# Kernel optimization log

Measured on AMD Instinct MI355X. Metric: run time of the kernel, lower is better.

## Reference

```python
import jax, jax.numpy as jnp
import numpy as np

N_NODES = 50000


def _gcn_conv(x, row, col, W, b, n_nodes):
    # symmetric-norm GCN conv with self loops already appended to (row, col)
    deg = jax.ops.segment_sum(jnp.ones_like(row, dtype=x.dtype), row, num_segments=n_nodes)
    # every node has a self loop, so deg >= 1; pow(-0.5) is finite
    dis = deg ** -0.5
    norm = dis[row] * dis[col]                       # [E']
    msg = x[row] * norm[:, None]                     # gather + scale  [E', d]
    agg = jax.ops.segment_sum(msg, col, num_segments=n_nodes)  # scatter-add [N, d]
    return agg @ W + b


def setup_inputs() -> dict:
    key = jax.random.key(0)
    ks = jax.random.split(key, 12)
    N, E, Q, d_in, h = N_NODES, 800000, 200000, 64, 128
    x = jax.random.normal(ks[0], (N, d_in), dtype=jnp.float32)
    edge_index = jax.random.randint(ks[1], (2, E), 0, N)
    edge_label_index = jax.random.randint(ks[2], (2, Q), 0, N)
    def lin(k, fan_in, fan_out):
        kw, kb = jax.random.split(k)
        bound = 1.0 / np.sqrt(fan_in)
        W = jax.random.uniform(kw, (fan_in, fan_out), minval=-bound, maxval=bound, dtype=jnp.float32)
        b = jax.random.uniform(kb, (fan_out,), minval=-bound, maxval=bound, dtype=jnp.float32)
        return W, b
    W1, b1 = lin(ks[3], d_in, h)
    W2, b2 = lin(ks[4], h, h)
    Wc1, bc1 = lin(ks[5], 2 * h, h)
    Wc2, bc2 = lin(ks[6], h, 1)
    return {"x": x, "edge_index": edge_index, "edge_label_index": edge_label_index,
            "W1": W1, "b1": b1, "W2": W2, "b2": b2,
            "Wc1": Wc1, "bc1": bc1, "Wc2": Wc2, "bc2": bc2}


def reference(x, edge_index, edge_label_index, W1, b1, W2, b2, Wc1, bc1, Wc2, bc2):
    n = x.shape[0]
    loops = jnp.arange(n, dtype=edge_index.dtype)
    row = jnp.concatenate([edge_index[0], loops])
    col = jnp.concatenate([edge_index[1], loops])
    h1 = jax.nn.relu(_gcn_conv(x, row, col, W1, b1, n))
    h2 = _gcn_conv(h1, row, col, W2, b2, n)
    src, dst = edge_label_index[0], edge_label_index[1]
    h = jnp.concatenate([h2[src], h2[dst]], axis=1)  # [Q, 2*hidden]
    h = jax.nn.relu(h @ Wc1 + bc1)
    return h @ Wc2 + bc2                              # [Q, 1]
```

## Files before the change

kernel.cpp:

```cpp
#include <hip/hip_runtime.h>


#define HB 64
#define NWIN 16384

typedef __attribute__((ext_vector_type(8))) short short8;
typedef __attribute__((ext_vector_type(4))) float floatx4;

static __device__ __forceinline__ unsigned int f2bf(float v) {
    union { float f; unsigned int u; } c; c.f = v;
    unsigned int lsb = (c.u >> 16) & 1u;
    c.u += 0x7FFFu + lsb;
    return c.u >> 16;
}
static __device__ __forceinline__ float bf2f(unsigned int h) {
    union { float f; unsigned int u; } c; c.u = h << 16;
    return c.f;
}

__global__ __launch_bounds__(256) void k_pre(const int* __restrict__ row,
                                             const int* __restrict__ col,
                                             unsigned int* __restrict__ hRow,
                                             unsigned int* __restrict__ hCol,
                                             const float* __restrict__ x,
                                             unsigned int* __restrict__ xb,
                                             const float* __restrict__ W1,
                                             const float* __restrict__ W2,
                                             const float* __restrict__ Wc1,
                                             const float* __restrict__ b2,
                                             const float* __restrict__ bc1,
                                             unsigned short* __restrict__ UVhi,
                                             unsigned short* __restrict__ UVlo,
                                             unsigned short* __restrict__ W1hi,
                                             unsigned short* __restrict__ W1lo,
                                             float* __restrict__ buv,
                                             int E, int N, int W, int chunk,
                                             int nHist, int nXb) {
    __shared__ unsigned int lds[NWIN];
    int t = threadIdx.x, b = blockIdx.x;
    if (b < nHist) {
        int hb = b % HB;
        int yb = b / HB;
        int p = yb >> 1, win = yb & 1;
        int base = win * NWIN;
        int wcap = min(W - base, NWIN);
        if (wcap <= 0) return;
        const int* idxArr = p ? col : row;
        unsigned int* outArr = p ? hCol : hRow;
        int e0 = hb * chunk, e1 = min(E, e0 + chunk);
        for (int i = t; i < wcap; i += 256) lds[i] = 0;
        __syncthreads();
        for (int e = e0 + t; e < e1; e += 256) {
            int idx = idxArr[e];
            int w = (idx >> 1) - base;
            if ((unsigned)w < (unsigned)wcap)
                atomicAdd(&lds[w], 1u << ((idx & 1) * 16));
        }
        __syncthreads();
        for (int i = t; i < wcap; i += 256)
            outArr[(size_t)hb * W + base + i] = lds[i];
    } else if (b < nHist + nXb) {
        int i = (b - nHist) * 256 + t;
        if (i < N * 32) {
            float2 v = ((const float2*)x)[i];
            xb[i] = f2bf(v.x) | (f2bf(v.y) << 16);
        }
    } else {
        int bf = b - nHist - nXb;
        float* w2row = (float*)lds;
        if (bf < 128) {
            int k = bf;
            int j = t & 127, half = t >> 7;
            int n = half * 128 + j;
            const float* wc = Wc1 + (size_t)half * 128 * 128 + j;
            if (t < 128) w2row[t] = W2[k * 128 + t];
            __syncthreads();
            float acc = 0.f;
#pragma unroll 8
            for (int m = 0; m < 128; m++) acc += w2row[m] * wc[(size_t)m * 128];
            int kstep = k >> 5, kl = k & 31, quad = kl >> 3, j8 = kl & 7;
            int nb = n >> 4, l = quad * 16 + (n & 15);
            int pidx = ((kstep * 16 + nb) * 64 + l) * 8 + j8;
            unsigned int h = f2bf(acc);
            UVhi[pidx] = (unsigned short)h;
            UVlo[pidx] = (unsigned short)f2bf(acc - bf2f(h));
        } else if (bf == 128) {
            int j = t & 127, half = t >> 7;
            const float* wc = Wc1 + (size_t)half * 128 * 128 + j;
            float acc = half ? 0.f : bc1[j];
#pragma unroll 8
            for (int m = 0; m < 128; m++) acc += b2[m] * wc[(size_t)m * 128];
            buv[half * 128 + j] = acc;
        } else {
            int idx = (bf - 129) * 256 + t;
            int k = idx >> 7, n = idx & 127;
            float v = W1[k * 128 + n];
            int kstep = k >> 5, kl = k & 31, quad = kl >> 3, j8 = kl & 7;
            int nb = n >> 4, l = quad * 16 + (n & 15);
            int pidx = ((kstep * 8 + nb) * 64 + l) * 8 + j8;
            unsigned int h = f2bf(v);
            W1hi[pidx] = (unsigned short)h;
            W1lo[pidx] = (unsigned short)f2bf(v - bf2f(h));
        }
    }
}

__global__ __launch_bounds__(256) void k_rs(const unsigned int* __restrict__ hRow,
                                            unsigned int* __restrict__ hCol,
                                            float* __restrict__ dis,
                                            int* __restrict__ offs,
                                            int* __restrict__ bsum,
                                            int N, int W) {
    __shared__ int ts[256];
    int t = threadIdx.x;
    int w = blockIdx.x * 256 + t;
    unsigned int r0 = 0, r1 = 0, c0 = 0, c1 = 0;
    if (w < W) {
#pragma unroll 8
        for (int b = 0; b < HB; b++) {
            size_t idx = (size_t)b * W + w;
            unsigned int hr = hRow[idx];
            unsigned int hc = hCol[idx];
            hCol[idx] = c0 | (c1 << 16);
            r0 += hr & 0xFFFFu; r1 += hr >> 16;
            c0 += hc & 0xFFFFu; c1 += hc >> 16;
        }
        int n0 = 2 * w, n1 = 2 * w + 1;
        dis[n0] = 1.0f / sqrtf((float)(r0 + 1));
        if (n1 < N) dis[n1] = 1.0f / sqrtf((float)(r1 + 1));
    }
    int sum = (w < W) ? (int)(c0 + c1) : 0;
    ts[t] = sum;
    __syncthreads();
    for (int off = 1; off < 256; off <<= 1) {
        int xv = (t >= off) ? ts[t - off] : 0;
        __syncthreads();
        ts[t] += xv;
        __syncthreads();
    }
    int e = ts[t] - sum;
    if (w < W) {
        int n0 = 2 * w, n1 = 2 * w + 1;
        offs[n0] = e;
        if (n1 < N) offs[n1] = e + (int)c0;
    }
    if (t == 255) bsum[blockIdx.x] = ts[255];
}

__global__ __launch_bounds__(256) void k_scan2(int* __restrict__ bsum, int B) {
    __shared__ int ts[256];
    int t = threadIdx.x;
    int v = (t < B) ? bsum[t] : 0;
    ts[t] = v;
    __syncthreads();
    for (int off = 1; off < 256; off <<= 1) {
        int x = (t >= off) ? ts[t - off] : 0;
        __syncthreads();
        ts[t] += x;
        __syncthreads();
    }
    if (t < B) bsum[t] = ts[t] - v;
}

__global__ __launch_bounds__(256) void k_scan3(int* __restrict__ offs,
                                               const int* __restrict__ bsum,
                                               int N, int E) {
    int i = blockIdx.x * 256 + threadIdx.x;
    if (i < N) offs[i] = offs[i] + bsum[i >> 9];
    if (i == 0) offs[N] = E;
}

__global__ __launch_bounds__(256) void k_fill3(const int* __restrict__ row,
                                               const int* __restrict__ col,
                                               const int* __restrict__ offs,
                                               const unsigned int* __restrict__ hCol,
                                               int* __restrict__ srcSorted,
                                               int E, int N, int W, int chunk) {
    __shared__ int base[NWIN];
    int t = threadIdx.x, b = blockIdx.x;
    int n0 = blockIdx.y * NWIN;
    int nCnt = min(NWIN, N - n0);
    int e0 = b * chunk, e1 = min(E, e0 + chunk);
    for (int wl = t; wl * 2 < nCnt; wl += 256) {
        unsigned int pref = hCol[(size_t)b * W + (n0 >> 1) + wl];
        int nn = n0 + wl * 2;
        base[wl * 2] = offs[nn] + (int)(pref & 0xFFFFu);
        if (wl * 2 + 1 < nCnt)
            base[wl * 2 + 1] = offs[nn + 1] + (int)(pref >> 16);
    }
    __syncthreads();
    for (int e = e0 + t; e < e1; e += 256) {
        int c = col[e] - n0;
        if ((unsigned)c < (unsigned)nCnt) {
            int pos = atomicAdd(&base[c], 1);
            srcSorted[pos] = row[e];
        }
    }
}

__global__ __launch_bounds__(256) void k_conv1(const unsigned short* __restrict__ s,
                                               const int* __restrict__ offs,
                                               const int* __restrict__ srcs,
                                               const float* __restrict__ dis,
                                               const unsigned short* __restrict__ Bhi,
                                               const unsigned short* __restrict__ Blo,
                                               const float* __restrict__ b1,
                                               unsigned short* __restrict__ h1b, int N) {
    __shared__ unsigned short Ahi[16][72];
    __shared__ unsigned short Alo[16][72];
    int t = threadIdx.x;
    int lane = t & 63, wave = t >> 6;
    int quad = lane >> 4;
    short8 bh[2][2], bl[2][2];
#pragma unroll
    for (int ks = 0; ks < 2; ks++)
#pragma unroll
        for (int nt = 0; nt < 2; nt++) {
            int nb = wave * 2 + nt;
            bh[ks][nt] = *(const short8*)(Bhi + ((ks * 8 + nb) * 64 + lane) * 8);
            bl[ks][nt] = *(const short8*)(Blo + ((ks * 8 + nb) * 64 + lane) * 8);
        }
    {
        int nl = t >> 4;
        int node = blockIdx.x * 16 + nl;
        if (node < N) {
            int c4 = (t & 15) * 4;
            int e = offs[node], eEnd = offs[node + 1];
            float dn = dis[node];
            uint2 w = *(const uint2*)(s + (size_t)node * 64 + c4);
            float4 acc;
            acc.x = bf2f(w.x & 0xFFFF) * dn; acc.y = bf2f(w.x >> 16) * dn;
            acc.z = bf2f(w.y & 0xFFFF) * dn; acc.w = bf2f(w.y >> 16) * dn;
            while (e + 1 < eEnd) {
                int sA = srcs[e], sB = srcs[e + 1];
                float dA = dis[sA], dB = dis[sB];
                uint2 vA = *(const uint2*)(s + (size_t)sA * 64 + c4);
                uint2 vB = *(const uint2*)(s + (size_t)sB * 64 + c4);
                acc.x += bf2f(vA.x & 0xFFFF) * dA + bf2f(vB.x & 0xFFFF) * dB;
                acc.y += bf2f(vA.x >> 16) * dA + bf2f(vB.x >> 16) * dB;
                acc.z += bf2f(vA.y & 0xFFFF) * dA + bf2f(vB.y & 0xFFFF) * dB;
                acc.w += bf2f(vA.y >> 16) * dA + bf2f(vB.y >> 16) * dB;
                e += 2;
            }
            if (e < eEnd) {
                int sA = srcs[e];
                float dA = dis[sA];
                uint2 vA = *(const uint2*)(s + (size_t)sA * 64 + c4);
                acc.x += bf2f(vA.x & 0xFFFF) * dA; acc.y += bf2f(vA.x >> 16) * dA;
                acc.z += bf2f(vA.y & 0xFFFF) * dA; acc.w += bf2f(vA.y >> 16) * dA;
            }
            acc.x *= dn; acc.y *= dn; acc.z *= dn; acc.w *= dn;
            unsigned int h0 = f2bf(acc.x), h1 = f2bf(acc.y),
                         h2 = f2bf(acc.z), h3 = f2bf(acc.w);
            uint2 hw; hw.x = h0 | (h1 << 16); hw.y = h2 | (h3 << 16);
            uint2 lw;
            lw.x = f2bf(acc.x - bf2f(h0)) | (f2bf(acc.y - bf2f(h1)) << 16);
            lw.y = f2bf(acc.z - bf2f(h2)) | (f2bf(acc.w - bf2f(h3)) << 16);
            *(uint2*)(&Ahi[nl][c4]) = hw;
            *(uint2*)(&Alo[nl][c4]) = lw;
        }
    }
    __syncthreads();
    int ml = lane & 15;
    floatx4 acc[2] = {};
#pragma unroll
    for (int ks = 0; ks < 2; ks++) {
        short8 ahi = *(const short8*)(&Ahi[ml][ks * 32 + quad * 8]);
        short8 alo = *(const short8*)(&Alo[ml][ks * 32 + quad * 8]);
#pragma unroll
        for (int nt = 0; nt < 2; nt++) {
            acc[nt] = __builtin_amdgcn_mfma_f32_16x16x32_bf16(ahi, bh[ks][nt], acc[nt], 0, 0, 0);
            acc[nt] = __builtin_amdgcn_mfma_f32_16x16x32_bf16(ahi, bl[ks][nt], acc[nt], 0, 0, 0);
            acc[nt] = __builtin_amdgcn_mfma_f32_16x16x32_bf16(alo, bh[ks][nt], acc[nt], 0, 0, 0);
        }
    }
    int md = blockIdx.x * 16 + quad * 4;
#pragma unroll
    for (int nt = 0; nt < 2; nt++) {
        int n0 = (wave * 2 + nt) * 16 + (lane & 15);
        float bias = b1[n0];
#pragma unroll
        for (int r = 0; r < 4; r++) {
            int node = md + r;
            if (node < N)
                h1b[(size_t)node * 128 + n0] =
                    (unsigned short)f2bf(fmaxf(acc[nt][r] + bias, 0.f) * dis[node]);
        }
    }
}

__global__ __launch_bounds__(512) void k_conv2(const unsigned short* __restrict__ s,
                                               const int* __restrict__ offs,
                                               const int* __restrict__ srcs,
                                               const float* __restrict__ dis,
                                               const unsigned short* __restrict__ Bhi,
                                               const unsigned short* __restrict__ Blo,
                                               const float* __restrict__ buv,
                                               unsigned short* __restrict__ Ub,
                                               unsigned short* __restrict__ Vb, int N) {
    __shared__ unsigned short Ab[32][136];
    int t = threadIdx.x;
    {
        int nl = t >> 4;
        int node = blockIdx.x * 32 + nl;
        int c8 = (t & 15) * 8;
        if (node < N) {
            int e = offs[node], eEnd = offs[node + 1];
            float dn = dis[node];
            uint4 w = *(const uint4*)(s + (size_t)node * 128 + c8);
            float a0 = bf2f(w.x & 0xFFFF), a1 = bf2f(w.x >> 16);
            float a2 = bf2f(w.y & 0xFFFF), a3 = bf2f(w.y >> 16);
            float a4 = bf2f(w.z & 0xFFFF), a5 = bf2f(w.z >> 16);
            float a6 = bf2f(w.w & 0xFFFF), a7 = bf2f(w.w >> 16);
            while (e + 1 < eEnd) {
                int sA = srcs[e], sB = srcs[e + 1];
                uint4 vA = *(const uint4*)(s + (size_t)sA * 128 + c8);
                uint4 vB = *(const uint4*)(s + (size_t)sB * 128 + c8);
                a0 += bf2f(vA.x & 0xFFFF) + bf2f(vB.x & 0xFFFF);
                a1 += bf2f(vA.x >> 16) + bf2f(vB.x >> 16);
                a2 += bf2f(vA.y & 0xFFFF) + bf2f(vB.y & 0xFFFF);
                a3 += bf2f(vA.y >> 16) + bf2f(vB.y >> 16);
                a4 += bf2f(vA.z & 0xFFFF) + bf2f(vB.z & 0xFFFF);
                a5 += bf2f(vA.z >> 16) + bf2f(vB.z >> 16);
                a6 += bf2f(vA.w & 0xFFFF) + bf2f(vB.w & 0xFFFF);
                a7 += bf2f(vA.w >> 16) + bf2f(vB.w >> 16);
                e += 2;
            }
            if (e < eEnd) {
                int sA = srcs[e];
                uint4 vA = *(const uint4*)(s + (size_t)sA * 128 + c8);
                a0 += bf2f(vA.x & 0xFFFF); a1 += bf2f(vA.x >> 16);
                a2 += bf2f(vA.y & 0xFFFF); a3 += bf2f(vA.y >> 16);
                a4 += bf2f(vA.z & 0xFFFF); a5 += bf2f(vA.z >> 16);
                a6 += bf2f(vA.w & 0xFFFF); a7 += bf2f(vA.w >> 16);
            }
            uint4 o;
            o.x = f2bf(a0 * dn) | (f2bf(a1 * dn) << 16);
            o.y = f2bf(a2 * dn) | (f2bf(a3 * dn) << 16);
            o.z = f2bf(a4 * dn) | (f2bf(a5 * dn) << 16);
            o.w = f2bf(a6 * dn) | (f2bf(a7 * dn) << 16);
            *(uint4*)(&Ab[nl][c8]) = o;
        } else {
            uint4 z; z.x = 0; z.y = 0; z.z = 0; z.w = 0;
            *(uint4*)(&Ab[nl][c8]) = z;
        }
    }
    int lane = t & 63, wave = t >> 6, quad = lane >> 4, ml = lane & 15;
    short8 bh[4][2], bl[4][2];
#pragma unroll
    for (int ks = 0; ks < 4; ks++)
#pragma unroll
        for (int nt = 0; nt < 2; nt++) {
            int nb = wave * 2 + nt;
            bh[ks][nt] = *(const short8*)(Bhi + ((ks * 16 + nb) * 64 + lane) * 8);
            bl[ks][nt] = *(const short8*)(Blo + ((ks * 16 + nb) * 64 + lane) * 8);
        }
    __syncthreads();
#pragma unroll
    for (int g = 0; g < 2; g++) {
        int mbase = blockIdx.x * 32 + g * 16;
        floatx4 acc[2] = {};
#pragma unroll
        for (int ks = 0; ks < 4; ks++) {
            short8 a = *(const short8*)(&Ab[g * 16 + ml][ks * 32 + quad * 8]);
#pragma unroll
            for (int nt = 0; nt < 2; nt++) {
                acc[nt] = __builtin_amdgcn_mfma_f32_16x16x32_bf16(a, bh[ks][nt], acc[nt], 0, 0, 0);
                acc[nt] = __builtin_amdgcn_mfma_f32_16x16x32_bf16(a, bl[ks][nt], acc[nt], 0, 0, 0);
            }
        }
        int md = mbase + quad * 4;
#pragma unroll
        for (int nt = 0; nt < 2; nt++) {
            int n0 = (wave * 2 + nt) * 16 + ml;
            float bias = buv[n0];
            unsigned short* dst = (n0 < 128) ? Ub : Vb;
            int cc = n0 & 127;
#pragma unroll
            for (int r = 0; r < 4; r++) {
                int nd = md + r;
                if (nd < N)
                    dst[(size_t)nd * 128 + cc] =
                        (unsigned short)f2bf(acc[nt][r] + bias);
            }
        }
    }
}

__global__ __launch_bounds__(256) void k_head(const unsigned short* __restrict__ Ub,
                                              const unsigned short* __restrict__ Vb,
                                              const int* __restrict__ srcA,
                                              const int* __restrict__ dstA,
                                              const float* __restrict__ Wc2,
                                              const float* __restrict__ bc2,
                                              float* __restrict__ out, int Q) {
    int t = threadIdx.x;
    int q = blockIdx.x * 16 + (t >> 4);
    if (q >= Q) return;
    int l = t & 15;
    int s = srcA[q], d = dstA[q];
    uint4 u = *(const uint4*)(Ub + (size_t)s * 128 + l * 8);
    uint4 v = *(const uint4*)(Vb + (size_t)d * 128 + l * 8);
    const float4* w = (const float4*)(Wc2 + l * 8);
    float4 w0 = w[0], w1 = w[1];
    float acc = 0.f, z;
    z = fmaxf(bf2f(u.x & 0xFFFF) + bf2f(v.x & 0xFFFF), 0.f); acc += z * w0.x;
    z = fmaxf(bf2f(u.x >> 16)    + bf2f(v.x >> 16),    0.f); acc += z * w0.y;
    z = fmaxf(bf2f(u.y & 0xFFFF) + bf2f(v.y & 0xFFFF), 0.f); acc += z * w0.z;
    z = fmaxf(bf2f(u.y >> 16)    + bf2f(v.y >> 16),    0.f); acc += z * w0.w;
    z = fmaxf(bf2f(u.z & 0xFFFF) + bf2f(v.z & 0xFFFF), 0.f); acc += z * w1.x;
    z = fmaxf(bf2f(u.z >> 16)    + bf2f(v.z >> 16),    0.f); acc += z * w1.y;
    z = fmaxf(bf2f(u.w & 0xFFFF) + bf2f(v.w & 0xFFFF), 0.f); acc += z * w1.z;
    z = fmaxf(bf2f(u.w >> 16)    + bf2f(v.w >> 16),    0.f); acc += z * w1.w;
    acc += __shfl_xor(acc, 1);
    acc += __shfl_xor(acc, 2);
    acc += __shfl_xor(acc, 4);
    acc += __shfl_xor(acc, 8);
    if (l == 0) out[q] = acc + bc2[0];
}

extern "C" void kernel_launch(void* const* d_in, const int* in_sizes, int n_in,
                              void* d_out, int out_size, void* d_ws, size_t ws_size,
                              hipStream_t stream) {
    const float* x   = (const float*)d_in[0];
    const int*   ei  = (const int*)d_in[1];
    const int*   eli = (const int*)d_in[2];
    const float* W1  = (const float*)d_in[3];
    const float* b1  = (const float*)d_in[4];
    const float* W2  = (const float*)d_in[5];
    const float* b2  = (const float*)d_in[6];
    const float* Wc1 = (const float*)d_in[7];
    const float* bc1 = (const float*)d_in[8];
    const float* Wc2 = (const float*)d_in[9];
    const float* bc2 = (const float*)d_in[10];
    float* out = (float*)d_out;
    char* wsb = (char*)d_ws;

    const int N = in_sizes[0] / 64;
    const int E = in_sizes[1] / 2;
    const int Q = in_sizes[2] / 2;
    const int W = (N + 1) / 2;
    const int chunk = (E + HB - 1) / HB;
    const int nPass = (N + NWIN - 1) / NWIN;
    const int nWinH = (W + NWIN - 1) / NWIN;
    const int nHist = HB * 2 * nWinH;
    const int nXb   = (N * 32 + 255) / 256;
    const int rsB   = (W + 255) / 256;

    float* dis       = (float*)wsb;
    int*   offs      = (int*)wsb + 65536;
    int*   bsum      = (int*)wsb + 197120;
    float* buv       = (float*)wsb + 262912;
    unsigned short* UVhi = (unsigned short*)((int*)wsb + 263168);
    unsigned short* UVlo = (unsigned short*)((int*)wsb + 279552);
    unsigned short* W1hi = (unsigned short*)((int*)wsb + 295936);
    unsigned short* W1lo = (unsigned short*)((int*)wsb + 300032);
    int*   srcSorted = (int*)wsb + 304128;
    unsigned short* Vb   = (unsigned short*)((int*)wsb + 1104128);
    unsigned short* h1b  = (unsigned short*)((int*)wsb + 4304128);
    unsigned short* Ub   = (unsigned short*)((int*)wsb + 7504128);
    unsigned int* hRow = (unsigned int*)wsb + 10704128;
    unsigned int* hCol = (unsigned int*)wsb + 12304128;
    unsigned int* xb   = (unsigned int*)wsb + 13904128;

    const int* row  = ei;
    const int* col  = ei + E;
    const int* srcA = eli;
    const int* dstA = eli + Q;

    k_pre<<<nHist + nXb + 161, 256, 0, stream>>>(
        row, col, hRow, hCol, x, xb, W1, W2, Wc1, b2, bc1,
        UVhi, UVlo, W1hi, W1lo, buv, E, N, W, chunk, nHist, nXb);
    k_rs<<<rsB, 256, 0, stream>>>(hRow, hCol, dis, offs, bsum, N, W);
    k_scan2<<<1, 256, 0, stream>>>(bsum, rsB);
    k_scan3<<<(N + 255) / 256, 256, 0, stream>>>(offs, bsum, N, E);
    k_fill3<<<dim3(HB, nPass), 256, 0, stream>>>(row, col, offs, hCol, srcSorted, E, N, W, chunk);
    k_conv1<<<(N + 15) / 16, 256, 0, stream>>>(
        (const unsigned short*)xb, offs, srcSorted, dis, W1hi, W1lo, b1, h1b, N);
    k_conv2<<<(N + 31) / 32, 512, 0, stream>>>(
        h1b, offs, srcSorted, dis, UVhi, UVlo, buv, Ub, Vb, N);
    k_head<<<(Q + 15) / 16, 256, 0, stream>>>(Ub, Vb, srcA, dstA, Wc2, bc2, out, Q);
}
```

Before: 257.9 us.

## Split conv2 neighbor gather across two half-warps and unroll gather loops by four

In conv2, each node's edge list is now split between two 16-lane groups that take alternating edges and combine their sums with a cross-lane shuffle. Each block handles 16 nodes instead of 32, so twice as many blocks launch. Conv1's gather loop is also unrolled to four edges per iteration. The goal is more gather loads in flight, to hide latency on the memory-bound aggregation. The cost is that each block loads the same B fragments from global memory twice as often, and work is duplicated when a node has few edges.

```diff
diff --git a/kernel.cpp b/kernel.cpp
--- a/kernel.cpp
+++ b/kernel.cpp
@@ -231,6 +231,23 @@
             float4 acc;
             acc.x = bf2f(w.x & 0xFFFF) * dn; acc.y = bf2f(w.x >> 16) * dn;
             acc.z = bf2f(w.y & 0xFFFF) * dn; acc.w = bf2f(w.y >> 16) * dn;
+            while (e + 3 < eEnd) {
+                int sA = srcs[e], sB = srcs[e + 1], sC = srcs[e + 2], sD = srcs[e + 3];
+                float dA = dis[sA], dB = dis[sB], dC = dis[sC], dD = dis[sD];
+                uint2 vA = *(const uint2*)(s + (size_t)sA * 64 + c4);
+                uint2 vB = *(const uint2*)(s + (size_t)sB * 64 + c4);
+                uint2 vC = *(const uint2*)(s + (size_t)sC * 64 + c4);
+                uint2 vD = *(const uint2*)(s + (size_t)sD * 64 + c4);
+                acc.x += bf2f(vA.x & 0xFFFF) * dA + bf2f(vB.x & 0xFFFF) * dB;
+                acc.y += bf2f(vA.x >> 16) * dA + bf2f(vB.x >> 16) * dB;
+                acc.z += bf2f(vA.y & 0xFFFF) * dA + bf2f(vB.y & 0xFFFF) * dB;
+                acc.w += bf2f(vA.y >> 16) * dA + bf2f(vB.y >> 16) * dB;
+                acc.x += bf2f(vC.x & 0xFFFF) * dC + bf2f(vD.x & 0xFFFF) * dD;
+                acc.y += bf2f(vC.x >> 16) * dC + bf2f(vD.x >> 16) * dD;
+                acc.z += bf2f(vC.y & 0xFFFF) * dC + bf2f(vD.y & 0xFFFF) * dD;
+                acc.w += bf2f(vC.y >> 16) * dC + bf2f(vD.y >> 16) * dD;
+                e += 4;
+            }
             while (e + 1 < eEnd) {
                 int sA = srcs[e], sB = srcs[e + 1];
                 float dA = dis[sA], dB = dis[sB];
@@ -298,54 +315,76 @@
                                                const float* __restrict__ buv,
                                                unsigned short* __restrict__ Ub,
                                                unsigned short* __restrict__ Vb, int N) {
-    __shared__ unsigned short Ab[32][136];
+    __shared__ unsigned short Ab[16][136];
     int t = threadIdx.x;
+    int lane = t & 63, wave = t >> 6;
     {
-        int nl = t >> 4;
-        int node = blockIdx.x * 32 + nl;
-        int c8 = (t & 15) * 8;
+        int nl = wave * 2 + (lane >> 5);
+        int node = blockIdx.x * 16 + nl;
+        int half = (lane >> 4) & 1;
+        int c8 = (lane & 15) * 8;
+        float a0 = 0.f, a1 = 0.f, a2 = 0.f, a3 = 0.f,
+              a4 = 0.f, a5 = 0.f, a6 = 0.f, a7 = 0.f;
+        float dn = 0.f;
         if (node < N) {
-            int e = offs[node], eEnd = offs[node + 1];
-            float dn = dis[node];
-            uint4 w = *(const uint4*)(s + (size_t)node * 128 + c8);
-            float a0 = bf2f(w.x & 0xFFFF), a1 = bf2f(w.x >> 16);
-            float a2 = bf2f(w.y & 0xFFFF), a3 = bf2f(w.y >> 16);
-            float a4 = bf2f(w.z & 0xFFFF), a5 = bf2f(w.z >> 16);
-            float a6 = bf2f(w.w & 0xFFFF), a7 = bf2f(w.w >> 16);
-            while (e + 1 < eEnd) {
-                int sA = srcs[e], sB = srcs[e + 1];
-                uint4 vA = *(const uint4*)(s + (size_t)sA * 128 + c8);
-                uint4 vB = *(const uint4*)(s + (size_t)sB * 128 + c8);
-                a0 += bf2f(vA.x & 0xFFFF) + bf2f(vB.x & 0xFFFF);
-                a1 += bf2f(vA.x >> 16) + bf2f(vB.x >> 16);
-                a2 += bf2f(vA.y & 0xFFFF) + bf2f(vB.y & 0xFFFF);
-                a3 += bf2f(vA.y >> 16) + bf2f(vB.y >> 16);
-                a4 += bf2f(vA.z & 0xFFFF) + bf2f(vB.z & 0xFFFF);
-                a5 += bf2f(vA.z >> 16) + bf2f(vB.z >> 16);
-                a6 += bf2f(vA.w & 0xFFFF) + bf2f(vB.w & 0xFFFF);
-                a7 += bf2f(vA.w >> 16) + bf2f(vB.w >> 16);
+            int eb = offs[node], eEnd = offs[node + 1];
+            dn = dis[node];
+            if (!half) {
+                uint4 w = *(const uint4*)(s + (size_t)node * 128 + c8);
+                a0 = bf2f(w.x & 0xFFFF); a1 = bf2f(w.x >> 16);
+                a2 = bf2f(w.y & 0xFFFF); a3 = bf2f(w.y >> 16);
+                a4 = bf2f(w.z & 0xFFFF); a5 = bf2f(w.z >> 16);
+                a6 = bf2f(w.w & 0xFFFF); a7 = bf2f(w.w >> 16);
+            }
+            int e = eb + half;
+            while (e + 6 < eEnd) {
+                int s0 = srcs[e], s1 = srcs[e + 2], s2 = srcs[e + 4], s3 = srcs[e + 6];
+                uint4 v0 = *(const uint4*)(s + (size_t)s0 * 128 + c8);
+                uint4 v1 = *(const uint4*)(s + (size_t)s1 * 128 + c8);
+                uint4 v2 = *(const uint4*)(s + (size_t)s2 * 128 + c8);
+                uint4 v3 = *(const uint4*)(s + (size_t)s3 * 128 + c8);
+                a0 += bf2f(v0.x & 0xFFFF) + bf2f(v1.x & 0xFFFF);
+                a1 += bf2f(v0.x >> 16) + bf2f(v1.x >> 16);
+                a2 += bf2f(v0.y & 0xFFFF) + bf2f(v1.y & 0xFFFF);
+                a3 += bf2f(v0.y >> 16) + bf2f(v1.y >> 16);
+                a4 += bf2f(v0.z & 0xFFFF) + bf2f(v1.z & 0xFFFF);
+                a5 += bf2f(v0.z >> 16) + bf2f(v1.z >> 16);
+                a6 += bf2f(v0.w & 0xFFFF) + bf2f(v1.w & 0xFFFF);
+                a7 += bf2f(v0.w >> 16) + bf2f(v1.w >> 16);
+                a0 += bf2f(v2.x & 0xFFFF) + bf2f(v3.x & 0xFFFF);
+                a1 += bf2f(v2.x >> 16) + bf2f(v3.x >> 16);
+                a2 += bf2f(v2.y & 0xFFFF) + bf2f(v3.y & 0xFFFF);
+                a3 += bf2f(v2.y >> 16) + bf2f(v3.y >> 16);
+                a4 += bf2f(v2.z & 0xFFFF) + bf2f(v3.z & 0xFFFF);
+                a5 += bf2f(v2.z >> 16) + bf2f(v3.z >> 16);
+                a6 += bf2f(v2.w & 0xFFFF) + bf2f(v3.w & 0xFFFF);
+                a7 += bf2f(v2.w >> 16) + bf2f(v3.w >> 16);
+                e += 8;
+            }
+            while (e < eEnd) {
+                int s0 = srcs[e];
+                uint4 v0 = *(const uint4*)(s + (size_t)s0 * 128 + c8);
+                a0 += bf2f(v0.x & 0xFFFF); a1 += bf2f(v0.x >> 16);
+                a2 += bf2f(v0.y & 0xFFFF); a3 += bf2f(v0.y >> 16);
+                a4 += bf2f(v0.z & 0xFFFF); a5 += bf2f(v0.z >> 16);
+                a6 += bf2f(v0.w & 0xFFFF); a7 += bf2f(v0.w >> 16);
                 e += 2;
             }
-            if (e < eEnd) {
-                int sA = srcs[e];
-                uint4 vA = *(const uint4*)(s + (size_t)sA * 128 + c8);
-                a0 += bf2f(vA.x & 0xFFFF); a1 += bf2f(vA.x >> 16);
-                a2 += bf2f(vA.y & 0xFFFF); a3 += bf2f(vA.y >> 16);
-                a4 += bf2f(vA.z & 0xFFFF); a5 += bf2f(vA.z >> 16);
-                a6 += bf2f(vA.w & 0xFFFF); a7 += bf2f(vA.w >> 16);
-            }
+        }
+        a0 += __shfl_xor(a0, 16); a1 += __shfl_xor(a1, 16);
+        a2 += __shfl_xor(a2, 16); a3 += __shfl_xor(a3, 16);
+        a4 += __shfl_xor(a4, 16); a5 += __shfl_xor(a5, 16);
+        a6 += __shfl_xor(a6, 16); a7 += __shfl_xor(a7, 16);
+        if (!half) {
             uint4 o;
             o.x = f2bf(a0 * dn) | (f2bf(a1 * dn) << 16);
             o.y = f2bf(a2 * dn) | (f2bf(a3 * dn) << 16);
             o.z = f2bf(a4 * dn) | (f2bf(a5 * dn) << 16);
             o.w = f2bf(a6 * dn) | (f2bf(a7 * dn) << 16);
             *(uint4*)(&Ab[nl][c8]) = o;
-        } else {
-            uint4 z; z.x = 0; z.y = 0; z.z = 0; z.w = 0;
-            *(uint4*)(&Ab[nl][c8]) = z;
-        }
-    }
-    int lane = t & 63, wave = t >> 6, quad = lane >> 4, ml = lane & 15;
+        }
+    }
+    int quad = lane >> 4, ml = lane & 15;
     short8 bh[4][2], bl[4][2];
 #pragma unroll
     for (int ks = 0; ks < 4; ks++)
@@ -356,33 +395,29 @@
             bl[ks][nt] = *(const short8*)(Blo + ((ks * 16 + nb) * 64 + lane) * 8);
         }
     __syncthreads();
-#pragma unroll
-    for (int g = 0; g < 2; g++) {
-        int mbase = blockIdx.x * 32 + g * 16;
-        floatx4 acc[2] = {};
-#pragma unroll
-        for (int ks = 0; ks < 4; ks++) {
-            short8 a = *(const short8*)(&Ab[g * 16 + ml][ks * 32 + quad * 8]);
-#pragma unroll
-            for (int nt = 0; nt < 2; nt++) {
-                acc[nt] = __builtin_amdgcn_mfma_f32_16x16x32_bf16(a, bh[ks][nt], acc[nt], 0, 0, 0);
-                acc[nt] = __builtin_amdgcn_mfma_f32_16x16x32_bf16(a, bl[ks][nt], acc[nt], 0, 0, 0);
-            }
-        }
-        int md = mbase + quad * 4;
+    floatx4 acc[2] = {};
+#pragma unroll
+    for (int ks = 0; ks < 4; ks++) {
+        short8 a = *(const short8*)(&Ab[ml][ks * 32 + quad * 8]);
 #pragma unroll
         for (int nt = 0; nt < 2; nt++) {
-            int n0 = (wave * 2 + nt) * 16 + ml;
-            float bias = buv[n0];
-            unsigned short* dst = (n0 < 128) ? Ub : Vb;
-            int cc = n0 & 127;
-#pragma unroll
-            for (int r = 0; r < 4; r++) {
-                int nd = md + r;
-                if (nd < N)
-                    dst[(size_t)nd * 128 + cc] =
-                        (unsigned short)f2bf(acc[nt][r] + bias);
-            }
+            acc[nt] = __builtin_amdgcn_mfma_f32_16x16x32_bf16(a, bh[ks][nt], acc[nt], 0, 0, 0);
+            acc[nt] = __builtin_amdgcn_mfma_f32_16x16x32_bf16(a, bl[ks][nt], acc[nt], 0, 0, 0);
+        }
+    }
+    int md = blockIdx.x * 16 + quad * 4;
+#pragma unroll
+    for (int nt = 0; nt < 2; nt++) {
+        int n0 = (wave * 2 + nt) * 16 + ml;
+        float bias = buv[n0];
+        unsigned short* dst = (n0 < 128) ? Ub : Vb;
+        int cc = n0 & 127;
+#pragma unroll
+        for (int r = 0; r < 4; r++) {
+            int nd = md + r;
+            if (nd < N)
+                dst[(size_t)nd * 128 + cc] =
+                    (unsigned short)f2bf(acc[nt][r] + bias);
         }
     }
 }
@@ -477,7 +512,7 @@
     k_fill3<<<dim3(HB, nPass), 256, 0, stream>>>(row, col, offs, hCol, srcSorted, E, N, W, chunk);
     k_conv1<<<(N + 15) / 16, 256, 0, stream>>>(
         (const unsigned short*)xb, offs, srcSorted, dis, W1hi, W1lo, b1, h1b, N);
-    k_conv2<<<(N + 31) / 32, 512, 0, stream>>>(
+    k_conv2<<<(N + 15) / 16, 512, 0, stream>>>(
         h1b, offs, srcSorted, dis, UVhi, UVlo, buv, Ub, Vb, N);
     k_head<<<(Q + 15) / 16, 256, 0, stream>>>(Ub, Vb, srcA, dstA, Wc2, bc2, out, Q);
 }
```

After: 261.3 us. Within noise of the previous version (+1.3%).
